# Kernel optimization log

Measured on AMD Instinct MI355X. Metric: run time of the kernel, lower is better.

Reference implementation:

```python
import jax, jax.numpy as jnp
import numpy as np

B, D, H = 8192, 256, 64


def setup_inputs() -> dict:
    key = jax.random.key(0)
    ks = jax.random.split(key, 7)
    noise = jax.random.normal(ks[0], (B, D), dtype=jnp.float32)
    adj_logits = jax.random.normal(ks[1], (D, D), dtype=jnp.float32) * 0.1
    # stacked per-node mechanism params: Linear(D,H) -> SiLU -> Linear(H,1)
    W1 = jax.random.normal(ks[2], (D, H, D), dtype=jnp.float32) * (1.0 / np.sqrt(D))
    b1 = jax.random.normal(ks[3], (D, H), dtype=jnp.float32) * (1.0 / np.sqrt(D))
    W2 = jax.random.normal(ks[4], (D, H), dtype=jnp.float32) * (1.0 / np.sqrt(H))
    b2 = jax.random.normal(ks[5], (D,), dtype=jnp.float32) * (1.0 / np.sqrt(H))
    log_sigma = jnp.zeros((D,), dtype=jnp.float32)  # torch init: tensor(0.0)
    return {"noise": noise, "adj_logits": adj_logits, "W1": W1, "b1": b1,
            "W2": W2, "b2": b2, "log_sigma": log_sigma}


def reference(noise, adj_logits, W1, b1, W2, b2, log_sigma):
    d = adj_logits.shape[0]
    # differentiable adjacency: sigmoid(logits) with zeroed diagonal
    adj = jax.nn.sigmoid(adj_logits) * (1.0 - jnp.eye(d, dtype=adj_logits.dtype))
    bsz = noise.shape[0]
    z0 = jnp.zeros((bsz, d), dtype=noise.dtype)

    def step(z, xs):
        i, a_col, w1, bb1, w2, bb2, ls, n_i = xs
        pv = z * a_col[None, :]                       # [B, D] masked parent values
        h = jax.nn.silu(pv @ w1.T + bb1[None, :])     # [B, H]
        det = h @ w2 + bb2                            # [B]
        val = det + jnp.exp(ls) * n_i                 # [B]
        z = jax.lax.dynamic_update_slice(z, val[:, None], (0, i))
        return z, None

    xs = (jnp.arange(d), adj.T, W1, b1, W2, b2, log_sigma, noise.T)
    z, _ = jax.lax.scan(step, z0, xs)
    return z
```

## Files before the change

kernel.cpp:

```cpp
#include <hip/hip_runtime.h>
#include <math.h>

#define Dn 256
#define Hn 64

typedef __attribute__((ext_vector_type(8))) short short8;
typedef float floatx4 __attribute__((ext_vector_type(4)));

static __device__ __forceinline__ unsigned short f2bf(float x) {
    unsigned int u = __float_as_uint(x);
    unsigned int r = (u + 0x7fffu + ((u >> 16) & 1u)) >> 16;
    return (unsigned short)r;
}

__global__ __launch_bounds__(256) void prep_sgm(const float* __restrict__ adj,
                                                float* __restrict__ sgm) {
    const int i = blockIdx.x, j = threadIdx.x;
    float m = 0.f;
    if (j != i) m = 1.f / (1.f + __expf(-adj[(size_t)j * Dn + i]));
    sgm[(size_t)i * Dn + j] = m;
}

__global__ __launch_bounds__(256) void prep_wb(const float* __restrict__ W1,
                                               const float* __restrict__ sgm,
                                               unsigned short* __restrict__ Wb) {
    const int c = blockIdx.x, i = blockIdx.y;
    const int t = threadIdx.x;
    const int nb = t >> 6, l = t & 63;
    const int kk = nb * 16 + (l & 15);
    const int jb = c * 32 + ((l >> 4) & 3) * 8;
    const float* wp = W1 + ((size_t)i * Hn + kk) * Dn + jb;
    const float* sp = sgm + (size_t)i * Dn + jb;
    unsigned short v[8];
#pragma unroll
    for (int e = 0; e < 8; ++e) v[e] = f2bf(wp[e] * sp[e]);
    unsigned short* dst = Wb + ((((size_t)i * 8 + c) * 4 + nb) * 64 + l) * 8;
    *(short8*)dst = *(const short8*)v;
}

__global__ __launch_bounds__(256) void prep_nst(const float* __restrict__ noise,
                                                const float* __restrict__ ls,
                                                float* __restrict__ nsT, int B) {
    __shared__ float tile[64][65];
    const int bi = blockIdx.x * 64, dj = blockIdx.y * 64;
    const int t = threadIdx.x, c = t & 63, rq = t >> 6;
#pragma unroll
    for (int it = 0; it < 16; ++it) {
        int b = bi + it * 4 + rq;
        tile[it * 4 + rq][c] = noise[(size_t)b * Dn + dj + c];
    }
    __syncthreads();
#pragma unroll
    for (int it = 0; it < 16; ++it) {
        int d = dj + it * 4 + rq;
        float sg = __expf(ls[d]);
        nsT[(size_t)d * B + bi + c] = tile[c][it * 4 + rq] * sg;
    }
}

__global__ __launch_bounds__(128, 1) void scm_main(const unsigned short* __restrict__ Wb,
                                                   const float* __restrict__ b1,
                                                   const float* __restrict__ W2,
                                                   const float* __restrict__ b2,
                                                   const float* __restrict__ nsT,
                                                   float* __restrict__ out, int B) {
    __shared__ unsigned short zbf[32][264];
    const int t = threadIdx.x;
    const int w = t >> 6, l = t & 63;
    const int n = l & 15, q = l >> 4;
    const int rowbase = blockIdx.x * 32 + w * 16;

    for (int idx = l; idx < 16 * 132; idx += 64) {
        int r = idx / 132, cc = idx - r * 132;
        ((unsigned int*)zbf[w * 16 + r])[cc] = 0u;
    }

    const unsigned short* wb_l = Wb + (size_t)l * 8;
    const unsigned short* zrow_lds = &zbf[w * 16 + n][0];

    short8 af[8];
    short8 bf[8][4];
    float b1v[4], w2v[4], b2v;
    float4 nv;

    {
#pragma unroll
        for (int nb = 0; nb < 4; ++nb) bf[0][nb] = *(const short8*)(wb_l + nb * 512);
#pragma unroll
        for (int nb = 0; nb < 4; ++nb) {
            b1v[nb] = b1[nb * 16 + n];
            w2v[nb] = W2[nb * 16 + n];
        }
        nv  = *(const float4*)(nsT + rowbase + q * 4);
        b2v = b2[0];
    }

#pragma unroll
    for (int sec = 0; sec < 8; ++sec) {
        if (sec > 0) {
            af[sec - 1] = *(const short8*)(zrow_lds + (sec - 1) * 32 + q * 8);
            const unsigned short* wbp = wb_l + (size_t)(sec * 32) * 16384 + sec * 2048;
#pragma unroll
            for (int nb = 0; nb < 4; ++nb) bf[sec][nb] = *(const short8*)(wbp + nb * 512);
        }
#pragma unroll 1
        for (int ii = 0; ii < 32; ++ii) {
            const int i = sec * 32 + ii;

            short8 ain = *(const short8*)(zrow_lds + sec * 32 + q * 8);

            floatx4 zero4 = {0.f, 0.f, 0.f, 0.f};
            floatx4 acc[4];
#pragma unroll
            for (int nb = 0; nb < 4; ++nb) acc[nb] = zero4;

#pragma unroll
            for (int c = 0; c < 8; ++c)
                if (c < sec) {
#pragma unroll
                    for (int nb = 0; nb < 4; ++nb)
                        acc[nb] = __builtin_amdgcn_mfma_f32_16x16x32_bf16(af[c], bf[c][nb], acc[nb], 0, 0, 0);
                }
#pragma unroll
            for (int nb = 0; nb < 4; ++nb)
                acc[nb] = __builtin_amdgcn_mfma_f32_16x16x32_bf16(ain, bf[sec][nb], acc[nb], 0, 0, 0);

            float b1c[4], w2c[4], nvr[4];
            float b2c = b2v;
#pragma unroll
            for (int nb = 0; nb < 4; ++nb) { b1c[nb] = b1v[nb]; w2c[nb] = w2v[nb]; }
            nvr[0] = nv.x; nvr[1] = nv.y; nvr[2] = nv.z; nvr[3] = nv.w;

            {
                int ip = i + 1; if (ip > 255) ip = 255;
                const unsigned short* wbp = wb_l + (size_t)ip * 16384;
#pragma unroll
                for (int c = 0; c < 8; ++c)
                    if (c <= sec) {
#pragma unroll
                        for (int nb = 0; nb < 4; ++nb)
                            bf[c][nb] = *(const short8*)(wbp + c * 2048 + nb * 512);
                    }
#pragma unroll
                for (int nb = 0; nb < 4; ++nb) {
                    b1v[nb] = b1[ip * Hn + nb * 16 + n];
                    w2v[nb] = W2[ip * Hn + nb * 16 + n];
                }
                nv  = *(const float4*)(nsT + (size_t)ip * B + rowbase + q * 4);
                b2v = b2[ip];
            }

            float d[4];
#pragma unroll
            for (int r = 0; r < 4; ++r) {
                float s = 0.f;
#pragma unroll
                for (int nb = 0; nb < 4; ++nb) {
                    float h = acc[nb][r] + b1c[nb];
                    s += __fdividef(h, 1.f + __expf(-h)) * w2c[nb];
                }
                d[r] = s;
            }
#pragma unroll
            for (int m = 1; m <= 8; m <<= 1) {
#pragma unroll
                for (int r = 0; r < 4; ++r) d[r] += __shfl_xor(d[r], m);
            }
            float z[4];
#pragma unroll
            for (int r = 0; r < 4; ++r) z[r] = d[r] + b2c + nvr[r];

            int srcl = ((l & 15) >> 2) << 4;
            float t0 = __shfl(z[0], srcl), t1 = __shfl(z[1], srcl);
            float t2 = __shfl(z[2], srcl), t3 = __shfl(z[3], srcl);
            float za = (l & 1) ? t1 : t0;
            float zb = (l & 1) ? t3 : t2;
            float zrow = (l & 2) ? zb : za;

            if (q == 0) {
                zbf[w * 16 + n][i] = f2bf(zrow);
                out[(size_t)(rowbase + n) * Dn + i] = zrow;
            }
        }
    }
}

extern "C" void kernel_launch(void* const* d_in, const int* in_sizes, int n_in,
                              void* d_out, int out_size, void* d_ws, size_t ws_size,
                              hipStream_t stream) {
    const float* noise      = (const float*)d_in[0];
    const float* adj_logits = (const float*)d_in[1];
    const float* W1         = (const float*)d_in[2];
    const float* b1         = (const float*)d_in[3];
    const float* W2         = (const float*)d_in[4];
    const float* b2         = (const float*)d_in[5];
    const float* log_sigma  = (const float*)d_in[6];
    float* out = (float*)d_out;

    const int B = in_sizes[0] / Dn;
    unsigned short* Wb  = (unsigned short*)d_ws;
    float*          nsT = (float*)((char*)d_ws + (size_t)Dn * Dn * Hn * 2);
    float*          sgm = nsT;

    prep_sgm<<<dim3(Dn), 256, 0, stream>>>(adj_logits, sgm);
    prep_wb<<<dim3(8, Dn), 256, 0, stream>>>(W1, sgm, Wb);
    prep_nst<<<dim3(B / 64, Dn / 64), 256, 0, stream>>>(noise, log_sigma, nsT, B);
    scm_main<<<dim3(B / 32), 128, 0, stream>>>(Wb, b1, W2, b2, nsT, out, B);
}
```

Measured before the change: 384.3 us.

## Stage per-step weight prefetch through double-buffered LDS via global_load_lds

Instead of prefetching the next node's bf16 W1 fragments into a large register array, each wave now issues direct global-to-LDS loads into a per-wave double buffer. MFMA B operands are read back from LDS, and an explicit vmcnt wait at the top of each step guards the buffer swap. The diagonal-section MFMA is skipped on the first step of each section, where those parent columns are still zero. This frees a large block of VGPRs held in flight, at the cost of extra LDS reads and a full memory wait every step.

```diff
diff --git a/kernel.cpp b/kernel.cpp
--- a/kernel.cpp
+++ b/kernel.cpp
@@ -11,6 +11,12 @@
     unsigned int u = __float_as_uint(x);
     unsigned int r = (u + 0x7fffu + ((u >> 16) & 1u)) >> 16;
     return (unsigned short)r;
+}
+
+static __device__ __forceinline__ void gll16(const unsigned short* g, unsigned short* l) {
+    __builtin_amdgcn_global_load_lds(
+        (const __attribute__((address_space(1))) unsigned int*)g,
+        (__attribute__((address_space(3))) unsigned int*)l, 16, 0, 0);
 }
 
 __global__ __launch_bounds__(256) void prep_sgm(const float* __restrict__ adj,
@@ -65,6 +71,7 @@
                                                    const float* __restrict__ nsT,
                                                    float* __restrict__ out, int B) {
     __shared__ unsigned short zbf[32][264];
+    __shared__ unsigned short wst[2][2][8][4][512];
     const int t = threadIdx.x;
     const int w = t >> 6, l = t & 63;
     const int n = l & 15, q = l >> 4;
@@ -75,17 +82,13 @@
         ((unsigned int*)zbf[w * 16 + r])[cc] = 0u;
     }
 
-    const unsigned short* wb_l = Wb + (size_t)l * 8;
     const unsigned short* zrow_lds = &zbf[w * 16 + n][0];
 
     short8 af[8];
-    short8 bf[8][4];
     float b1v[4], w2v[4], b2v;
     float4 nv;
 
     {
-#pragma unroll
-        for (int nb = 0; nb < 4; ++nb) bf[0][nb] = *(const short8*)(wb_l + nb * 512);
 #pragma unroll
         for (int nb = 0; nb < 4; ++nb) {
             b1v[nb] = b1[nb * 16 + n];
@@ -99,31 +102,13 @@
     for (int sec = 0; sec < 8; ++sec) {
         if (sec > 0) {
             af[sec - 1] = *(const short8*)(zrow_lds + (sec - 1) * 32 + q * 8);
-            const unsigned short* wbp = wb_l + (size_t)(sec * 32) * 16384 + sec * 2048;
-#pragma unroll
-            for (int nb = 0; nb < 4; ++nb) bf[sec][nb] = *(const short8*)(wbp + nb * 512);
         }
 #pragma unroll 1
         for (int ii = 0; ii < 32; ++ii) {
             const int i = sec * 32 + ii;
-
-            short8 ain = *(const short8*)(zrow_lds + sec * 32 + q * 8);
-
-            floatx4 zero4 = {0.f, 0.f, 0.f, 0.f};
-            floatx4 acc[4];
-#pragma unroll
-            for (int nb = 0; nb < 4; ++nb) acc[nb] = zero4;
-
-#pragma unroll
-            for (int c = 0; c < 8; ++c)
-                if (c < sec) {
-#pragma unroll
-                    for (int nb = 0; nb < 4; ++nb)
-                        acc[nb] = __builtin_amdgcn_mfma_f32_16x16x32_bf16(af[c], bf[c][nb], acc[nb], 0, 0, 0);
-                }
-#pragma unroll
-            for (int nb = 0; nb < 4; ++nb)
-                acc[nb] = __builtin_amdgcn_mfma_f32_16x16x32_bf16(ain, bf[sec][nb], acc[nb], 0, 0, 0);
+            const int p = ii & 1;
+
+            asm volatile("s_waitcnt vmcnt(0)" ::: "memory");
 
             float b1c[4], w2c[4], nvr[4];
             float b2c = b2v;
@@ -133,13 +118,13 @@
 
             {
                 int ip = i + 1; if (ip > 255) ip = 255;
-                const unsigned short* wbp = wb_l + (size_t)ip * 16384;
+                const unsigned short* wrow = Wb + (size_t)ip * 16384 + l * 8;
 #pragma unroll
                 for (int c = 0; c < 8; ++c)
                     if (c <= sec) {
 #pragma unroll
                         for (int nb = 0; nb < 4; ++nb)
-                            bf[c][nb] = *(const short8*)(wbp + c * 2048 + nb * 512);
+                            gll16(wrow + c * 2048 + nb * 512, &wst[1 - p][w][c][nb][0]);
                     }
 #pragma unroll
                 for (int nb = 0; nb < 4; ++nb) {
@@ -148,6 +133,29 @@
                 }
                 nv  = *(const float4*)(nsT + (size_t)ip * B + rowbase + q * 4);
                 b2v = b2[ip];
+            }
+
+            floatx4 zero4 = {0.f, 0.f, 0.f, 0.f};
+            floatx4 acc[4];
+#pragma unroll
+            for (int nb = 0; nb < 4; ++nb) acc[nb] = zero4;
+
+#pragma unroll
+            for (int c = 0; c < 8; ++c)
+                if (c < sec) {
+#pragma unroll
+                    for (int nb = 0; nb < 4; ++nb) {
+                        short8 bfr = *(const short8*)&wst[p][w][c][nb][l * 8];
+                        acc[nb] = __builtin_amdgcn_mfma_f32_16x16x32_bf16(af[c], bfr, acc[nb], 0, 0, 0);
+                    }
+                }
+            if (ii != 0) {
+                short8 ain = *(const short8*)(zrow_lds + sec * 32 + q * 8);
+#pragma unroll
+                for (int nb = 0; nb < 4; ++nb) {
+                    short8 bfr = *(const short8*)&wst[p][w][sec][nb][l * 8];
+                    acc[nb] = __builtin_amdgcn_mfma_f32_16x16x32_bf16(ain, bfr, acc[nb], 0, 0, 0);
+                }
             }
 
             float d[4];
```

After: 538.6 us. 40.1% more time.

## Keep latent z in registers via transposed MFMA, dropping LDS round-trip

Applied to the files above, without the earlier changes.

Swaps the MFMA operand order so the output is transposed: each lane ends up owning one batch row's value. The latent z then stays as packed bf16 in a register vector instead of going through LDS. The epilogue reduction shrinks to two cross-lane shuffles, and the final row-gather shuffles go away. The current section is accumulated separately from the finished earlier sections, and empty asm pins keep the prefetched weights live. This shortens the serial per-step dependency chain (LDS write/read, shuffles), at the cost of extra register pressure and some wasted lanes on the select-merge update.

```diff
diff --git a/kernel.cpp b/kernel.cpp
--- a/kernel.cpp
+++ b/kernel.cpp
@@ -5,7 +5,10 @@
 #define Hn 64
 
 typedef __attribute__((ext_vector_type(8))) short short8;
-typedef float floatx4 __attribute__((ext_vector_type(4)));
+typedef __attribute__((ext_vector_type(4))) float floatx4;
+typedef __attribute__((ext_vector_type(4))) unsigned int uint4v;
+
+#define PIN(x) asm volatile("" :: "v"(x))
 
 static __device__ __forceinline__ unsigned short f2bf(float x) {
     unsigned int u = __float_as_uint(x);
@@ -64,123 +67,120 @@
                                                    const float* __restrict__ b2,
                                                    const float* __restrict__ nsT,
                                                    float* __restrict__ out, int B) {
-    __shared__ unsigned short zbf[32][264];
     const int t = threadIdx.x;
     const int w = t >> 6, l = t & 63;
     const int n = l & 15, q = l >> 4;
     const int rowbase = blockIdx.x * 32 + w * 16;
 
-    for (int idx = l; idx < 16 * 132; idx += 64) {
-        int r = idx / 132, cc = idx - r * 132;
-        ((unsigned int*)zbf[w * 16 + r])[cc] = 0u;
-    }
-
     const unsigned short* wb_l = Wb + (size_t)l * 8;
-    const unsigned short* zrow_lds = &zbf[w * 16 + n][0];
 
     short8 af[8];
-    short8 bf[8][4];
-    float b1v[4], w2v[4], b2v;
-    float4 nv;
-
-    {
-#pragma unroll
-        for (int nb = 0; nb < 4; ++nb) bf[0][nb] = *(const short8*)(wb_l + nb * 512);
-#pragma unroll
-        for (int nb = 0; nb < 4; ++nb) {
-            b1v[nb] = b1[nb * 16 + n];
-            w2v[nb] = W2[nb * 16 + n];
-        }
-        nv  = *(const float4*)(nsT + rowbase + q * 4);
-        b2v = b2[0];
-    }
+    short8 wf[8][4];
+    uint4v ain = {0u, 0u, 0u, 0u};
+    floatx4 b1v[4], w2v[4];
+    float nvv, b2v;
+
+#pragma unroll
+    for (int nb = 0; nb < 4; ++nb) {
+        b1v[nb] = *(const floatx4*)(b1 + nb * 16 + q * 4);
+        w2v[nb] = *(const floatx4*)(W2 + nb * 16 + q * 4);
+    }
+    nvv = nsT[rowbase + n];
+    b2v = b2[0];
 
 #pragma unroll
     for (int sec = 0; sec < 8; ++sec) {
         if (sec > 0) {
-            af[sec - 1] = *(const short8*)(zrow_lds + (sec - 1) * 32 + q * 8);
-            const unsigned short* wbp = wb_l + (size_t)(sec * 32) * 16384 + sec * 2048;
-#pragma unroll
-            for (int nb = 0; nb < 4; ++nb) bf[sec][nb] = *(const short8*)(wbp + nb * 512);
+            af[sec - 1] = __builtin_bit_cast(short8, ain);
+            ain = (uint4v){0u, 0u, 0u, 0u};
         }
 #pragma unroll 1
         for (int ii = 0; ii < 32; ++ii) {
             const int i = sec * 32 + ii;
 
-            short8 ain = *(const short8*)(zrow_lds + sec * 32 + q * 8);
-
-            floatx4 zero4 = {0.f, 0.f, 0.f, 0.f};
-            floatx4 acc[4];
-#pragma unroll
-            for (int nb = 0; nb < 4; ++nb) acc[nb] = zero4;
-
+            floatx4 aA[4], aB[4];
+#pragma unroll
+            for (int nb = 0; nb < 4; ++nb) {
+                aA[nb] = (floatx4){0.f, 0.f, 0.f, 0.f};
+                aB[nb] = (floatx4){0.f, 0.f, 0.f, 0.f};
+            }
+
+            if (ii != 0) {
+                short8 zi = __builtin_bit_cast(short8, ain);
+#pragma unroll
+                for (int nb = 0; nb < 4; ++nb)
+                    aB[nb] = __builtin_amdgcn_mfma_f32_16x16x32_bf16(wf[sec][nb], zi, aB[nb], 0, 0, 0);
+            }
 #pragma unroll
             for (int c = 0; c < 8; ++c)
                 if (c < sec) {
 #pragma unroll
                     for (int nb = 0; nb < 4; ++nb)
-                        acc[nb] = __builtin_amdgcn_mfma_f32_16x16x32_bf16(af[c], bf[c][nb], acc[nb], 0, 0, 0);
-                }
-#pragma unroll
-            for (int nb = 0; nb < 4; ++nb)
-                acc[nb] = __builtin_amdgcn_mfma_f32_16x16x32_bf16(ain, bf[sec][nb], acc[nb], 0, 0, 0);
-
-            float b1c[4], w2c[4], nvr[4];
-            float b2c = b2v;
+                        aA[nb] = __builtin_amdgcn_mfma_f32_16x16x32_bf16(wf[c][nb], af[c], aA[nb], 0, 0, 0);
+                }
+
+            floatx4 b1c[4], w2c[4];
+            float nvc = nvv, b2c = b2v;
 #pragma unroll
             for (int nb = 0; nb < 4; ++nb) { b1c[nb] = b1v[nb]; w2c[nb] = w2v[nb]; }
-            nvr[0] = nv.x; nvr[1] = nv.y; nvr[2] = nv.z; nvr[3] = nv.w;
 
             {
                 int ip = i + 1; if (ip > 255) ip = 255;
-                const unsigned short* wbp = wb_l + (size_t)ip * 16384;
+                const unsigned short* wp = wb_l + (size_t)ip * 16384;
 #pragma unroll
                 for (int c = 0; c < 8; ++c)
                     if (c <= sec) {
 #pragma unroll
                         for (int nb = 0; nb < 4; ++nb)
-                            bf[c][nb] = *(const short8*)(wbp + c * 2048 + nb * 512);
+                            wf[c][nb] = *(const short8*)(wp + c * 2048 + nb * 512);
                     }
 #pragma unroll
                 for (int nb = 0; nb < 4; ++nb) {
-                    b1v[nb] = b1[ip * Hn + nb * 16 + n];
-                    w2v[nb] = W2[ip * Hn + nb * 16 + n];
-                }
-                nv  = *(const float4*)(nsT + (size_t)ip * B + rowbase + q * 4);
+                    b1v[nb] = *(const floatx4*)(b1 + ip * Hn + nb * 16 + q * 4);
+                    w2v[nb] = *(const floatx4*)(W2 + ip * Hn + nb * 16 + q * 4);
+                }
+                nvv = nsT[(size_t)ip * B + rowbase + n];
                 b2v = b2[ip];
             }
 
-            float d[4];
-#pragma unroll
-            for (int r = 0; r < 4; ++r) {
-                float s = 0.f;
-#pragma unroll
-                for (int nb = 0; nb < 4; ++nb) {
-                    float h = acc[nb][r] + b1c[nb];
-                    s += __fdividef(h, 1.f + __expf(-h)) * w2c[nb];
-                }
-                d[r] = s;
-            }
-#pragma unroll
-            for (int m = 1; m <= 8; m <<= 1) {
-#pragma unroll
-                for (int r = 0; r < 4; ++r) d[r] += __shfl_xor(d[r], m);
-            }
-            float z[4];
-#pragma unroll
-            for (int r = 0; r < 4; ++r) z[r] = d[r] + b2c + nvr[r];
-
-            int srcl = ((l & 15) >> 2) << 4;
-            float t0 = __shfl(z[0], srcl), t1 = __shfl(z[1], srcl);
-            float t2 = __shfl(z[2], srcl), t3 = __shfl(z[3], srcl);
-            float za = (l & 1) ? t1 : t0;
-            float zb = (l & 1) ? t3 : t2;
-            float zrow = (l & 2) ? zb : za;
-
-            if (q == 0) {
-                zbf[w * 16 + n][i] = f2bf(zrow);
-                out[(size_t)(rowbase + n) * Dn + i] = zrow;
-            }
+            float s = 0.f;
+#pragma unroll
+            for (int nb = 0; nb < 4; ++nb) {
+#pragma unroll
+                for (int r = 0; r < 4; ++r) {
+                    float h = (aA[nb][r] + aB[nb][r]) + b1c[nb][r];
+                    s += __fdividef(h, 1.f + __expf(-h)) * w2c[nb][r];
+                }
+            }
+            s += __shfl_xor(s, 16);
+            s += __shfl_xor(s, 32);
+            float z = s + b2c + nvc;
+
+            {
+                unsigned int zb = (unsigned int)f2bf(z);
+                unsigned int sh = (unsigned int)(ii & 1) << 4;
+                unsigned int val = zb << sh;
+                unsigned int msk = 0xFFFFu << sh;
+                const int own = (q == (ii >> 3));
+                const int wsel = (ii >> 1) & 3;
+#pragma unroll
+                for (int wd = 0; wd < 4; ++wd) {
+                    unsigned int merged = (ain[wd] & ~msk) | val;
+                    ain[wd] = (own && (wsel == wd)) ? merged : ain[wd];
+                }
+            }
+
+            if (q == 0) out[(size_t)(rowbase + n) * Dn + i] = z;
+
+#pragma unroll
+            for (int c = 0; c < 8; ++c)
+                if (c <= sec) {
+#pragma unroll
+                    for (int nb = 0; nb < 4; ++nb) PIN(wf[c][nb]);
+                }
+#pragma unroll
+            for (int nb = 0; nb < 4; ++nb) { PIN(b1v[nb]); PIN(w2v[nb]); }
+            PIN(nvv); PIN(b2v);
         }
     }
 }
```

Result: slower. 402.2 us (+4.7%).
